# Performance work log

Measured on AMD Instinct MI355X. Metric: run time of the kernel, lower is better.

## Reference

```python
import jax, jax.numpy as jnp
import numpy as np

HIDDEN = 256
GAMMA = 0.96875
SCALE_BASE = 512


def _rotate_every_two(x):
    x1 = x[..., ::2]
    x2 = x[..., 1::2]
    return jnp.stack((-x2, x1), axis=-1).reshape(x.shape)


def _xpos(x, downscale):
    # x: [B, H, L, D]; offset=0 path of XPOS._forward_impl
    L = x.shape[2]
    D = x.shape[-1]
    half = D // 2
    # buffer: (arange(0, D, 2) + 0.4*D) / (1.4*D)  -> [half]
    scale_vec = (jnp.arange(0, D, 2, dtype=jnp.float32) + 0.4 * D) / (1.4 * D)
    # scale ** (arange(L)/scale_base)[:, None] -> [L, half]
    exps = jnp.arange(L, dtype=jnp.float32) / SCALE_BASE
    scale = scale_vec[None, :] ** exps[:, None]
    # fixed_pos_embedding on scale (dim = half)
    inv_freq = 1.0 / (10000.0 ** (jnp.arange(half, dtype=jnp.float32) / half))
    sinusoid = jnp.arange(L, dtype=jnp.float32)[:, None] * inv_freq[None, :]  # [L, half]
    sin = jnp.sin(sinusoid)
    cos = jnp.cos(sinusoid)
    if downscale:
        scale = 1.0 / scale
    sin2 = jnp.repeat(sin * scale, 2, axis=-1)  # duplicate_interleave -> [L, D]
    cos2 = jnp.repeat(cos * scale, 2, axis=-1)
    return x * cos2 + _rotate_every_two(x) * sin2


def _decay_mask(L):
    n = jnp.arange(L)[:, None]
    m = jnp.arange(L)[None, :]
    return jnp.where(n >= m, jnp.power(GAMMA, (n - m).astype(jnp.float32)), 0.0)


def setup_inputs() -> dict:
    key = jax.random.key(0)
    k1, k2, k3, k4 = jax.random.split(key, 4)
    B, H, L, D = 8, 4, 2048, HIDDEN
    X = jax.random.normal(k1, (B, H, L, D), dtype=jnp.float32)
    W_Q = jax.random.normal(k2, (D, D), dtype=jnp.float32) / D
    W_K = jax.random.normal(k3, (D, D), dtype=jnp.float32) / D
    W_V = jax.random.normal(k4, (D, D), dtype=jnp.float32) / D
    return {"X": X, "W_Q": W_Q, "W_K": W_K, "W_V": W_V}


def reference(X, W_Q, W_K, W_V):
    L = X.shape[2]
    Q = X @ W_Q
    K = X @ W_K
    Q = _xpos(Q, downscale=False)
    K = _xpos(K, downscale=True)
    V = X @ W_V
    D = _decay_mask(L)  # [L, L]
    att = jnp.einsum('bhnd,bhmd->bhnm', Q, K) * D[None, None]
    return att @ V
```

## Files before the change

### kernel.cpp

```cpp
#include <hip/hip_runtime.h>
#include <stdint.h>

typedef unsigned short u16;
typedef unsigned int   u32;
typedef __attribute__((ext_vector_type(8))) short  bf16x8;
typedef __attribute__((ext_vector_type(4))) float  f32x4;
typedef __attribute__((ext_vector_type(4))) u32    u32x4;
typedef __attribute__((ext_vector_type(2))) u32    u32x2;

#define L_SEQ 2048
#define DMODEL 256

__device__ __forceinline__ u16 f2bf(float x){
  u32 u = __float_as_uint(x);
  return (u16)((u + 0x7FFFu + ((u >> 16) & 1u)) >> 16);
}

__device__ __forceinline__ u32 pack2(float a, float b){
  return (u32)f2bf(a) | ((u32)f2bf(b) << 16);
}

__device__ __forceinline__ void gload_lds16(const void* g, void* l){
  __builtin_amdgcn_global_load_lds(
      (const __attribute__((address_space(1))) u32*)g,
      (__attribute__((address_space(3))) u32*)l, 16, 0, 0);
}

__global__ void k_tables(float2* __restrict__ tq2, float2* __restrict__ tk2){
  int idx = blockIdx.x * 256 + threadIdx.x;
  int n = idx >> 7, hi = idx & 127;
  float fn = (float)n, fi = (float)hi;
  float invf = exp2f(-(fi * (1.0f/128.0f)) * 13.2877124f);
  float ang = fn * invf;
  float s = sinf(ang), c = cosf(ang);
  float sv = (2.0f * fi + 102.4f) * (1.0f / 358.4f);
  float sc = exp2f((fn * (1.0f/512.0f)) * log2f(sv));
  float2 q; q.x = c * sc;  q.y = s * sc;
  tq2[idx] = q;
  float inv = 1.0f / sc;
  float2 k; k.x = c * inv; k.y = s * inv;
  tk2[idx] = k;
}

__global__ void k_wt(const float* __restrict__ wq, const float* __restrict__ wk,
                     const float* __restrict__ wv, u16* __restrict__ wt2){
  int idx = blockIdx.x * 256 + threadIdx.x;
  int kc = idx / 6144, r = idx % 6144;
  int col = r >> 3, p = r & 7;
  int j = p ^ (col & 7);
  int wsel = col >> 8, c = col & 255;
  const float* src = (wsel == 0) ? wq : ((wsel == 1) ? wk : wv);
  int k0 = kc * 64 + j * 8;
  u32x4 v;
  v.x = pack2(src[(k0+0)*256 + c], src[(k0+1)*256 + c]);
  v.y = pack2(src[(k0+2)*256 + c], src[(k0+3)*256 + c]);
  v.z = pack2(src[(k0+4)*256 + c], src[(k0+5)*256 + c]);
  v.w = pack2(src[(k0+6)*256 + c], src[(k0+7)*256 + c]);
  *(u32x4*)(wt2 + (size_t)idx * 8) = v;
}

__global__ void k_xbf(const float* __restrict__ X, u16* __restrict__ Xb2){
  int idx = blockIdx.x * 256 + threadIdx.x;
  int row = idx >> 5, g = idx & 31;
  int kc = g >> 3, j = g & 7;
  int p = j ^ (row & 7);
  const float4* src = (const float4*)(X + (size_t)row * 256 + g * 8);
  float4 a = src[0], b = src[1];
  u32x4 v;
  v.x = pack2(a.x, a.y); v.y = pack2(a.z, a.w);
  v.z = pack2(b.x, b.y); v.w = pack2(b.z, b.w);
  *(u32x4*)(Xb2 + (((size_t)kc * 65536 + row) * 8 + p) * 8) = v;
}

__global__ __launch_bounds__(256, 2) void k_proj(
    const u16* __restrict__ Xb2, const u16* __restrict__ Wt2,
    const float2* __restrict__ tq2, const float2* __restrict__ tk2,
    u16* __restrict__ Qx, u16* __restrict__ Kx, u16* __restrict__ VT)
{
  __shared__ char smem[65536];
  const int p0 = blockIdx.x;
  const int l = (p0 & 7) * 384 + (p0 >> 3);
  const int ct = l % 6;
  const int rt = l / 6;
  const int wsel = ct >> 1;
  const int mcol0 = (ct & 1) * 128;
  const int row0 = rt * 128;
  const int bh = rt >> 4;
  const int tid = threadIdx.x;
  const int lane = tid & 63, wid = tid >> 6;
  const int h = lane >> 4, l15 = lane & 15;
  const int wrg = wid >> 1, wcg = wid & 1;

  f32x4 acc[4][4] = {};

  auto stage = [&](int kc, int buf){
    const u16* xsrc = Xb2 + ((size_t)kc * 65536 + row0) * 64;
    const u16* wsrc = Wt2 + ((size_t)kc * 768 + ct * 128) * 64;
    char* xdst = smem + buf * 16384;
    char* wdst = smem + 32768 + buf * 16384;
#pragma unroll
    for (int t = 0; t < 4; ++t){
      int ci = t * 256 + tid;
      gload_lds16(xsrc + ci * 8, xdst + (t * 256 + wid * 64) * 16);
      gload_lds16(wsrc + ci * 8, wdst + (t * 256 + wid * 64) * 16);
    }
  };

  stage(0, 0);
  __syncthreads();

  for (int kc = 0; kc < 4; ++kc){
    const int cur = kc & 1;
    if (kc < 3) stage(kc + 1, cur ^ 1);

    const char* lX = smem + cur * 16384;
    const char* lW = smem + 32768 + cur * 16384;
#pragma unroll
    for (int kb = 0; kb < 2; ++kb){
      bf16x8 xf[4], wf[4];
#pragma unroll
      for (int b = 0; b < 4; ++b){
        int r = wrg * 64 + b * 16 + l15;
        int p = (kb * 4 + h) ^ (r & 7);
        xf[b] = *(const bf16x8*)(lX + r * 128 + p * 16);
      }
#pragma unroll
      for (int a = 0; a < 4; ++a){
        int c = wcg * 64 + a * 16 + l15;
        int p = (kb * 4 + h) ^ (c & 7);
        wf[a] = *(const bf16x8*)(lW + c * 128 + p * 16);
      }
      if (wsel < 2){
#pragma unroll
        for (int a = 0; a < 4; ++a)
#pragma unroll
          for (int b = 0; b < 4; ++b)
            acc[a][b] = __builtin_amdgcn_mfma_f32_16x16x32_bf16(
                wf[a], xf[b], acc[a][b], 0, 0, 0);
      } else {
#pragma unroll
        for (int b = 0; b < 4; ++b)
#pragma unroll
          for (int a = 0; a < 4; ++a)
            acc[b][a] = __builtin_amdgcn_mfma_f32_16x16x32_bf16(
                xf[b], wf[a], acc[b][a], 0, 0, 0);
      }
    }
    __syncthreads();
  }

  if (wsel < 2){
    const float2* tt = (wsel == 0) ? tq2 : tk2;
    u16* Od = (wsel == 0) ? Qx : Kx;
#pragma unroll
    for (int a = 0; a < 4; ++a){
      int d0 = mcol0 + wcg * 64 + a * 16 + h * 4;
#pragma unroll
      for (int b = 0; b < 4; ++b){
        int n = row0 + wrg * 64 + b * 16 + l15;
        int pos = n & 2047;
        f32x4 v = acc[a][b];
        float4 t = *(const float4*)(tt + pos * 128 + (d0 >> 1));
        float y0 = v.x * t.x - v.y * t.y;
        float y1 = v.y * t.x + v.x * t.y;
        float y2 = v.z * t.z - v.w * t.w;
        float y3 = v.w * t.z + v.z * t.w;
        u32x2 p2; p2.x = pack2(y0, y1); p2.y = pack2(y2, y3);
        int lrow = wrg * 64 + b * 16 + l15;
        int lcolb = (wcg * 64 + a * 16 + h * 4) * 2;
        *(u32x2*)(smem + lrow * 256 + (lcolb ^ ((lrow & 7) << 4))) = p2;
      }
    }
    __syncthreads();
    {
      const int r = tid >> 1;
      const int cbase = (tid & 1) * 8;
      u16* orow = Od + (size_t)(row0 + r) * 256 + mcol0 + cbase * 8;
#pragma unroll
      for (int j = 0; j < 8; ++j){
        int c16 = cbase + j;
        u32x4 v = *(const u32x4*)(smem + r * 256 +
                                  ((c16 * 16) ^ ((r & 7) << 4)));
        *(u32x4*)(orow + j * 8) = v;
      }
    }
  } else {
#pragma unroll
    for (int b = 0; b < 4; ++b){
      int lpos = wrg * 64 + b * 16 + h * 4;
#pragma unroll
      for (int a = 0; a < 4; ++a){
        int ld = wcg * 64 + a * 16 + l15;
        f32x4 v = acc[b][a];
        u32x2 p2; p2.x = pack2(v.x, v.y); p2.y = pack2(v.z, v.w);
        *(u32x2*)(smem + ld * 256 + ((lpos * 2) ^ ((ld & 7) << 4))) = p2;
      }
    }
    __syncthreads();
    {
      const int dloc = tid >> 1;
      const int cbase = (tid & 1) * 8;
      const int posbase = (rt & 15) * 128;
      u16* orow = VT + ((size_t)bh * DMODEL + mcol0 + dloc) * 2048 +
                  posbase + cbase * 8;
#pragma unroll
      for (int j = 0; j < 8; ++j){
        int c16 = cbase + j;
        u32x4 v = *(const u32x4*)(smem + dloc * 256 +
                                  ((c16 * 16) ^ ((dloc & 7) << 4)));
        *(u32x4*)(orow + j * 8) = v;
      }
    }
  }
}

__global__ __launch_bounds__(512) void k_attn(
    const u16* __restrict__ Qx, const u16* __restrict__ Kx,
    const u16* __restrict__ VT, float* __restrict__ out)
{
  __shared__ char smem[131072];

  const int pbid = blockIdx.x;
  const int bid = ((pbid & 7) << 6) | (pbid >> 3);
  const int bh = bid >> 4, i = bid & 15;
  const int tid = threadIdx.x;
  const int lane = tid & 63, w = tid >> 6;
  const int h = lane >> 4, l15 = lane & 15;
  const int n_g = i * 128 + w * 16 + l15;

  bf16x8 q[8];
  const u16* qbase = Qx + ((size_t)bh * 2048 + n_g) * 256;
#pragma unroll
  for (int kb = 0; kb < 8; ++kb)
    q[kb] = *(const bf16x8*)(qbase + kb * 32 + h * 8);

  f32x4 ot[16] = {};

  int j_lo = 2 * i - 4; if (j_lo < 0) j_lo = 0;
  const int j_hi = 2 * i + 1;
  const float L2G = -0.04580369f;
  const float GI1 = 1.03225806f;
  const float GI2 = 1.06555671f;
  const float GI3 = 1.09993040f;

  auto stage = [&](int j, int buf){
    const u16* kbase = Kx + ((size_t)bh * 2048 + j * 64) * 256;
    char* kdst = smem + buf * 32768;
#pragma unroll
    for (int t = 0; t < 4; ++t){
      int s = (w * 4 + t) * 64 + lane;
      int m = s >> 5, c = s & 31;
      gload_lds16(kbase + m * 256 + ((c ^ (m & 7)) * 8),
                  kdst + (w * 4 + t) * 1024);
    }
    const u16* vbase = VT + (size_t)bh * (DMODEL * 2048) + j * 64;
    char* vdst = smem + 65536 + buf * 32768;
#pragma unroll
    for (int t = 0; t < 4; ++t){
      int s = (w * 4 + t) * 64 + lane;
      int d = s >> 3, c = s & 7;
      gload_lds16(vbase + (size_t)d * 2048 + ((c ^ (d & 7)) * 8),
                  vdst + (w * 4 + t) * 1024);
    }
  };

  stage(j_lo, 0);
  __syncthreads();

  for (int j = j_lo; j <= j_hi; ++j){
    const int cur = (j - j_lo) & 1;
    if (j < j_hi) stage(j + 1, cur ^ 1);

    if (i * 128 + w * 16 + 15 >= j * 64){
      const char* ldsK = smem + cur * 32768;
      const char* ldsV = smem + 65536 + cur * 32768;
      f32x4 sacc[4] = {};
#pragma unroll
      for (int kb = 0; kb < 8; ++kb){
#pragma unroll
        for (int mt = 0; mt < 4; ++mt){
          int m = mt * 16 + l15;
          int chunk = kb * 4 + h;
          bf16x8 a = *(const bf16x8*)(ldsK + m * 512 +
                                      ((chunk ^ (m & 7)) * 16));
          sacc[mt] = __builtin_amdgcn_mfma_f32_16x16x32_bf16(
              a, q[kb], sacc[mt], 0, 0, 0);
        }
      }
      u32 dA[4], dB[4];
#pragma unroll
      for (int mt = 0; mt < 4; ++mt){
        int m0 = j * 64 + mt * 16 + h * 4;
        int dl = n_g - m0;
        float base = exp2f((float)dl * L2G);
        float v0 = (dl     >= 0) ? sacc[mt].x * base       : 0.0f;
        float v1 = (dl - 1 >= 0) ? sacc[mt].y * base * GI1 : 0.0f;
        float v2 = (dl - 2 >= 0) ? sacc[mt].z * base * GI2 : 0.0f;
        float v3 = (dl - 3 >= 0) ? sacc[mt].w * base * GI3 : 0.0f;
        dA[mt] = pack2(v0, v1);
        dB[mt] = pack2(v2, v3);
      }
      int s0 = l15 + 32 * (h & 1);
      int s1 = s0 + 16;
      bool lo = (h < 2);
#pragma unroll
      for (int kt = 0; kt < 2; ++kt){
        u32 a0 = (u32)__shfl((int)dA[2 * kt],     s0, 64);
        u32 a1 = (u32)__shfl((int)dA[2 * kt + 1], s0, 64);
        u32 b0 = (u32)__shfl((int)dB[2 * kt],     s0, 64);
        u32 b1 = (u32)__shfl((int)dB[2 * kt + 1], s0, 64);
        u32 a2 = (u32)__shfl((int)dA[2 * kt],     s1, 64);
        u32 a3 = (u32)__shfl((int)dA[2 * kt + 1], s1, 64);
        u32 b2 = (u32)__shfl((int)dB[2 * kt],     s1, 64);
        u32 b3 = (u32)__shfl((int)dB[2 * kt + 1], s1, 64);
        union { u32 u[4]; bf16x8 v; } uu;
        uu.u[0] = lo ? a0 : a1;
        uu.u[1] = lo ? b0 : b1;
        uu.u[2] = lo ? a2 : a3;
        uu.u[3] = lo ? b2 : b3;
        bf16x8 bfrag = uu.v;
#pragma unroll
        for (int dt = 0; dt < 16; ++dt){
          int d = dt * 16 + l15;
          int chunk = kt * 4 + h;
          bf16x8 a = *(const bf16x8*)(ldsV + d * 128 +
                                      ((chunk ^ (d & 7)) * 16));
          ot[dt] = __builtin_amdgcn_mfma_f32_16x16x32_bf16(
              a, bfrag, ot[dt], 0, 0, 0);
        }
      }
    }
    __syncthreads();
  }

  float* obase = out + ((size_t)bh * 2048 + n_g) * 256;
#pragma unroll
  for (int dt = 0; dt < 16; ++dt)
    *(f32x4*)(obase + dt * 16 + h * 4) = ot[dt];
}

extern "C" void kernel_launch(void* const* d_in, const int* in_sizes, int n_in,
                              void* d_out, int out_size, void* d_ws, size_t ws_size,
                              hipStream_t stream)
{
  (void)in_sizes; (void)n_in; (void)out_size; (void)ws_size;
  const float* X  = (const float*)d_in[0];
  const float* WQ = (const float*)d_in[1];
  const float* WK = (const float*)d_in[2];
  const float* WV = (const float*)d_in[3];
  float* out = (float*)d_out;

  char* ws = (char*)d_ws;
  float2* tq2 = (float2*)ws;
  float2* tk2 = (float2*)(ws + (2u << 20));
  u16* wt2 = (u16*)(ws + (4u << 20));
  u16* qx = (u16*)(ws + 4718592);
  u16* kx = (u16*)(ws + 38273024);
  u16* vt = (u16*)(ws + 71827456);

  u16* xb2 = (u16*)d_out;

  k_tables<<<dim3(1024), dim3(256), 0, stream>>>(tq2, tk2);
  k_wt<<<dim3(96), dim3(256), 0, stream>>>(WQ, WK, WV, wt2);
  k_xbf<<<dim3(8192), dim3(256), 0, stream>>>(X, xb2);
  k_proj<<<dim3(3072), dim3(256), 0, stream>>>(xb2, wt2, tq2, tk2, qx, kx, vt);
  k_attn<<<dim3(512), dim3(512), 0, stream>>>(qx, kx, vt, out);
}
```

Baseline: 143.8 us.

## Keep X tile resident in LDS and compute Q, K, V projections per block

The projection kernel now launches one 512-thread block per 128-row tile. The block loads the full 128x256 X tile into LDS once and loops over the Q, K and V weight matrices, streaming double-buffered 256-column weight chunks, instead of having six blocks each reload X for one 128-column slice. This removes redundant X reads from global memory but uses 128KB of LDS and leaves far fewer blocks for latency hiding. Separately, the attention kernel raises wave priority around its MFMA loops with s_setprio.

```diff
diff --git a/kernel.cpp b/kernel.cpp
--- a/kernel.cpp
+++ b/kernel.cpp
@@ -72,145 +72,150 @@
   *(u32x4*)(Xb2 + (((size_t)kc * 65536 + row) * 8 + p) * 8) = v;
 }
 
-__global__ __launch_bounds__(256, 2) void k_proj(
+__global__ __launch_bounds__(512, 2) void k_proj(
     const u16* __restrict__ Xb2, const u16* __restrict__ Wt2,
     const float2* __restrict__ tq2, const float2* __restrict__ tk2,
     u16* __restrict__ Qx, u16* __restrict__ Kx, u16* __restrict__ VT)
 {
-  __shared__ char smem[65536];
-  const int p0 = blockIdx.x;
-  const int l = (p0 & 7) * 384 + (p0 >> 3);
-  const int ct = l % 6;
-  const int rt = l / 6;
-  const int wsel = ct >> 1;
-  const int mcol0 = (ct & 1) * 128;
+  __shared__ char smem[131072];
+  const int rt = blockIdx.x;
   const int row0 = rt * 128;
   const int bh = rt >> 4;
   const int tid = threadIdx.x;
   const int lane = tid & 63, wid = tid >> 6;
   const int h = lane >> 4, l15 = lane & 15;
-  const int wrg = wid >> 1, wcg = wid & 1;
-
-  f32x4 acc[4][4] = {};
-
-  auto stage = [&](int kc, int buf){
+  const int wrg = wid >> 2, wcg = wid & 3;
+
+  char* const E = smem + 65536;
+
+  auto stageW = [&](int wsel, int kc, int buf){
+    const u16* wsrc = Wt2 + ((size_t)kc * 768 + wsel * 256) * 64;
+    char* dst = E + buf * 32768;
+#pragma unroll
+    for (int t = 0; t < 4; ++t){
+      int ci = t * 512 + tid;
+      gload_lds16(wsrc + ci * 8, dst + (t * 512 + wid * 64) * 16);
+    }
+  };
+
+#pragma unroll
+  for (int kc = 0; kc < 4; ++kc){
     const u16* xsrc = Xb2 + ((size_t)kc * 65536 + row0) * 64;
-    const u16* wsrc = Wt2 + ((size_t)kc * 768 + ct * 128) * 64;
-    char* xdst = smem + buf * 16384;
-    char* wdst = smem + 32768 + buf * 16384;
-#pragma unroll
-    for (int t = 0; t < 4; ++t){
-      int ci = t * 256 + tid;
-      gload_lds16(xsrc + ci * 8, xdst + (t * 256 + wid * 64) * 16);
-      gload_lds16(wsrc + ci * 8, wdst + (t * 256 + wid * 64) * 16);
-    }
-  };
-
-  stage(0, 0);
+#pragma unroll
+    for (int t = 0; t < 2; ++t){
+      int ci = t * 512 + tid;
+      gload_lds16(xsrc + ci * 8, smem + kc * 16384 + (t * 512 + wid * 64) * 16);
+    }
+  }
+  stageW(0, 0, 0);
   __syncthreads();
 
-  for (int kc = 0; kc < 4; ++kc){
-    const int cur = kc & 1;
-    if (kc < 3) stage(kc + 1, cur ^ 1);
-
-    const char* lX = smem + cur * 16384;
-    const char* lW = smem + 32768 + cur * 16384;
-#pragma unroll
-    for (int kb = 0; kb < 2; ++kb){
-      bf16x8 xf[4], wf[4];
+#pragma unroll
+  for (int wsel = 0; wsel < 3; ++wsel){
+    f32x4 acc[4][4] = {};
+
+    for (int kc = 0; kc < 4; ++kc){
+      const int cur = kc & 1;
+      if (kc < 3) stageW(wsel, kc + 1, cur ^ 1);
+      const char* lX = smem + kc * 16384;
+      const char* lW = E + cur * 32768;
+#pragma unroll
+      for (int kb = 0; kb < 2; ++kb){
+        bf16x8 xf[4], wf[4];
+#pragma unroll
+        for (int b = 0; b < 4; ++b){
+          int r = wrg * 64 + b * 16 + l15;
+          int p = (kb * 4 + h) ^ (r & 7);
+          xf[b] = *(const bf16x8*)(lX + r * 128 + p * 16);
+        }
+#pragma unroll
+        for (int a = 0; a < 4; ++a){
+          int c = wcg * 64 + a * 16 + l15;
+          int p = (kb * 4 + h) ^ (c & 7);
+          wf[a] = *(const bf16x8*)(lW + c * 128 + p * 16);
+        }
+        if (wsel < 2){
+#pragma unroll
+          for (int a = 0; a < 4; ++a)
+#pragma unroll
+            for (int b = 0; b < 4; ++b)
+              acc[a][b] = __builtin_amdgcn_mfma_f32_16x16x32_bf16(
+                  wf[a], xf[b], acc[a][b], 0, 0, 0);
+        } else {
+#pragma unroll
+          for (int b = 0; b < 4; ++b)
+#pragma unroll
+            for (int a = 0; a < 4; ++a)
+              acc[b][a] = __builtin_amdgcn_mfma_f32_16x16x32_bf16(
+                  xf[b], wf[a], acc[b][a], 0, 0, 0);
+        }
+      }
+      __syncthreads();
+    }
+
+    if (wsel < 2){
+      const float2* tt = (wsel == 0) ? tq2 : tk2;
+      u16* Od = (wsel == 0) ? Qx : Kx;
+#pragma unroll
+      for (int a = 0; a < 4; ++a){
+        int d0 = wcg * 64 + a * 16 + h * 4;
+#pragma unroll
+        for (int b = 0; b < 4; ++b){
+          int n = row0 + wrg * 64 + b * 16 + l15;
+          int pos = n & 2047;
+          f32x4 v = acc[a][b];
+          float4 t = *(const float4*)(tt + pos * 128 + (d0 >> 1));
+          float y0 = v.x * t.x - v.y * t.y;
+          float y1 = v.y * t.x + v.x * t.y;
+          float y2 = v.z * t.z - v.w * t.w;
+          float y3 = v.w * t.z + v.z * t.w;
+          u32x2 p2; p2.x = pack2(y0, y1); p2.y = pack2(y2, y3);
+          int lrow = wrg * 64 + b * 16 + l15;
+          *(u32x2*)(E + lrow * 512 + ((d0 * 2) ^ ((lrow & 7) << 4))) = p2;
+        }
+      }
+      __syncthreads();
+      {
+        const int r = tid >> 2;
+        const int q4 = tid & 3;
+        u16* orow = Od + (size_t)(row0 + r) * 256 + q4 * 64;
+#pragma unroll
+        for (int j = 0; j < 8; ++j){
+          int c = q4 * 8 + j;
+          u32x4 v = *(const u32x4*)(E + r * 512 +
+                                    ((c * 16) ^ ((r & 7) << 4)));
+          *(u32x4*)(orow + j * 8) = v;
+        }
+      }
+    } else {
 #pragma unroll
       for (int b = 0; b < 4; ++b){
-        int r = wrg * 64 + b * 16 + l15;
-        int p = (kb * 4 + h) ^ (r & 7);
-        xf[b] = *(const bf16x8*)(lX + r * 128 + p * 16);
-      }
-#pragma unroll
-      for (int a = 0; a < 4; ++a){
-        int c = wcg * 64 + a * 16 + l15;
-        int p = (kb * 4 + h) ^ (c & 7);
-        wf[a] = *(const bf16x8*)(lW + c * 128 + p * 16);
-      }
-      if (wsel < 2){
-#pragma unroll
-        for (int a = 0; a < 4; ++a)
-#pragma unroll
-          for (int b = 0; b < 4; ++b)
-            acc[a][b] = __builtin_amdgcn_mfma_f32_16x16x32_bf16(
-                wf[a], xf[b], acc[a][b], 0, 0, 0);
-      } else {
-#pragma unroll
-        for (int b = 0; b < 4; ++b)
-#pragma unroll
-          for (int a = 0; a < 4; ++a)
-            acc[b][a] = __builtin_amdgcn_mfma_f32_16x16x32_bf16(
-                xf[b], wf[a], acc[b][a], 0, 0, 0);
+        int lpos = wrg * 64 + b * 16 + h * 4;
+#pragma unroll
+        for (int a = 0; a < 4; ++a){
+          int ld = wcg * 64 + a * 16 + l15;
+          f32x4 v = acc[b][a];
+          u32x2 p2; p2.x = pack2(v.x, v.y); p2.y = pack2(v.z, v.w);
+          *(u32x2*)(E + ld * 256 + ((lpos * 2) ^ ((ld & 7) << 4))) = p2;
+        }
+      }
+      __syncthreads();
+      {
+        const int d = tid >> 1;
+        const int half = tid & 1;
+        u16* orow = VT + ((size_t)bh * DMODEL + d) * 2048 +
+                    (rt & 15) * 128 + half * 64;
+#pragma unroll
+        for (int j = 0; j < 8; ++j){
+          int c = half * 8 + j;
+          u32x4 v = *(const u32x4*)(E + d * 256 +
+                                    ((c * 16) ^ ((d & 7) << 4)));
+          *(u32x4*)(orow + j * 8) = v;
+        }
       }
     }
     __syncthreads();
-  }
-
-  if (wsel < 2){
-    const float2* tt = (wsel == 0) ? tq2 : tk2;
-    u16* Od = (wsel == 0) ? Qx : Kx;
-#pragma unroll
-    for (int a = 0; a < 4; ++a){
-      int d0 = mcol0 + wcg * 64 + a * 16 + h * 4;
-#pragma unroll
-      for (int b = 0; b < 4; ++b){
-        int n = row0 + wrg * 64 + b * 16 + l15;
-        int pos = n & 2047;
-        f32x4 v = acc[a][b];
-        float4 t = *(const float4*)(tt + pos * 128 + (d0 >> 1));
-        float y0 = v.x * t.x - v.y * t.y;
-        float y1 = v.y * t.x + v.x * t.y;
-        float y2 = v.z * t.z - v.w * t.w;
-        float y3 = v.w * t.z + v.z * t.w;
-        u32x2 p2; p2.x = pack2(y0, y1); p2.y = pack2(y2, y3);
-        int lrow = wrg * 64 + b * 16 + l15;
-        int lcolb = (wcg * 64 + a * 16 + h * 4) * 2;
-        *(u32x2*)(smem + lrow * 256 + (lcolb ^ ((lrow & 7) << 4))) = p2;
-      }
-    }
-    __syncthreads();
-    {
-      const int r = tid >> 1;
-      const int cbase = (tid & 1) * 8;
-      u16* orow = Od + (size_t)(row0 + r) * 256 + mcol0 + cbase * 8;
-#pragma unroll
-      for (int j = 0; j < 8; ++j){
-        int c16 = cbase + j;
-        u32x4 v = *(const u32x4*)(smem + r * 256 +
-                                  ((c16 * 16) ^ ((r & 7) << 4)));
-        *(u32x4*)(orow + j * 8) = v;
-      }
-    }
-  } else {
-#pragma unroll
-    for (int b = 0; b < 4; ++b){
-      int lpos = wrg * 64 + b * 16 + h * 4;
-#pragma unroll
-      for (int a = 0; a < 4; ++a){
-        int ld = wcg * 64 + a * 16 + l15;
-        f32x4 v = acc[b][a];
-        u32x2 p2; p2.x = pack2(v.x, v.y); p2.y = pack2(v.z, v.w);
-        *(u32x2*)(smem + ld * 256 + ((lpos * 2) ^ ((ld & 7) << 4))) = p2;
-      }
-    }
-    __syncthreads();
-    {
-      const int dloc = tid >> 1;
-      const int cbase = (tid & 1) * 8;
-      const int posbase = (rt & 15) * 128;
-      u16* orow = VT + ((size_t)bh * DMODEL + mcol0 + dloc) * 2048 +
-                  posbase + cbase * 8;
-#pragma unroll
-      for (int j = 0; j < 8; ++j){
-        int c16 = cbase + j;
-        u32x4 v = *(const u32x4*)(smem + dloc * 256 +
-                                  ((c16 * 16) ^ ((dloc & 7) << 4)));
-        *(u32x4*)(orow + j * 8) = v;
-      }
-    }
+    if (wsel < 2){ stageW(wsel + 1, 0, 0); __syncthreads(); }
   }
 }
 
@@ -275,6 +280,7 @@
       const char* ldsK = smem + cur * 32768;
       const char* ldsV = smem + 65536 + cur * 32768;
       f32x4 sacc[4] = {};
+      __builtin_amdgcn_s_setprio(1);
 #pragma unroll
       for (int kb = 0; kb < 8; ++kb){
 #pragma unroll
@@ -287,6 +293,7 @@
               a, q[kb], sacc[mt], 0, 0, 0);
         }
       }
+      __builtin_amdgcn_s_setprio(0);
       u32 dA[4], dB[4];
 #pragma unroll
       for (int mt = 0; mt < 4; ++mt){
@@ -319,6 +326,7 @@
         uu.u[2] = lo ? a2 : a3;
         uu.u[3] = lo ? b2 : b3;
         bf16x8 bfrag = uu.v;
+        __builtin_amdgcn_s_setprio(1);
 #pragma unroll
         for (int dt = 0; dt < 16; ++dt){
           int d = dt * 16 + l15;
@@ -328,6 +336,7 @@
           ot[dt] = __builtin_amdgcn_mfma_f32_16x16x32_bf16(
               a, bfrag, ot[dt], 0, 0, 0);
         }
+        __builtin_amdgcn_s_setprio(0);
       }
     }
     __syncthreads();
@@ -363,6 +372,6 @@
   k_tables<<<dim3(1024), dim3(256), 0, stream>>>(tq2, tk2);
   k_wt<<<dim3(96), dim3(256), 0, stream>>>(WQ, WK, WV, wt2);
   k_xbf<<<dim3(8192), dim3(256), 0, stream>>>(X, xb2);
-  k_proj<<<dim3(3072), dim3(256), 0, stream>>>(xb2, wt2, tq2, tk2, qx, kx, vt);
+  k_proj<<<dim3(512), dim3(512), 0, stream>>>(xb2, wt2, tq2, tk2, qx, kx, vt);
   k_attn<<<dim3(512), dim3(512), 0, stream>>>(qx, kx, vt, out);
 }
```

Result: slower. 157.7 us (+9.7%).

## Shrink projection K-chunks to 32 for higher occupancy; add MFMA priority in attention

Applied to the files above, without the earlier changes.

The projection kernel now stages 32-wide K chunks instead of 64, halving its LDS footprint to 32 KB. This raises the launch-bounds occupancy hint from 2 to 5 blocks. The pre-pass kernels re-pack X and the weights to match the new 4-chunk swizzle layout. The attention kernel wraps its MFMA loops in s_setprio to favour matrix issue over other waves. The cost is twice as many sync/stage iterations in the projection kernel, plus possible register pressure from the tighter bound.

```diff
diff --git a/kernel.cpp b/kernel.cpp
--- a/kernel.cpp
+++ b/kernel.cpp
@@ -43,41 +43,41 @@
 }
 
 __global__ void k_wt(const float* __restrict__ wq, const float* __restrict__ wk,
-                     const float* __restrict__ wv, u16* __restrict__ wt2){
+                     const float* __restrict__ wv, u16* __restrict__ wt3){
   int idx = blockIdx.x * 256 + threadIdx.x;
-  int kc = idx / 6144, r = idx % 6144;
-  int col = r >> 3, p = r & 7;
-  int j = p ^ (col & 7);
+  int kc = idx / 3072, r = idx % 3072;
+  int col = r >> 2, p = r & 3;
+  int j = p ^ ((col >> 1) & 3);
   int wsel = col >> 8, c = col & 255;
   const float* src = (wsel == 0) ? wq : ((wsel == 1) ? wk : wv);
-  int k0 = kc * 64 + j * 8;
+  int k0 = kc * 32 + j * 8;
   u32x4 v;
   v.x = pack2(src[(k0+0)*256 + c], src[(k0+1)*256 + c]);
   v.y = pack2(src[(k0+2)*256 + c], src[(k0+3)*256 + c]);
   v.z = pack2(src[(k0+4)*256 + c], src[(k0+5)*256 + c]);
   v.w = pack2(src[(k0+6)*256 + c], src[(k0+7)*256 + c]);
-  *(u32x4*)(wt2 + (size_t)idx * 8) = v;
-}
-
-__global__ void k_xbf(const float* __restrict__ X, u16* __restrict__ Xb2){
+  *(u32x4*)(wt3 + (size_t)idx * 8) = v;
+}
+
+__global__ void k_xbf(const float* __restrict__ X, u16* __restrict__ Xb3){
   int idx = blockIdx.x * 256 + threadIdx.x;
   int row = idx >> 5, g = idx & 31;
-  int kc = g >> 3, j = g & 7;
-  int p = j ^ (row & 7);
+  int kc = g >> 2, j = g & 3;
+  int p = j ^ ((row >> 1) & 3);
   const float4* src = (const float4*)(X + (size_t)row * 256 + g * 8);
   float4 a = src[0], b = src[1];
   u32x4 v;
   v.x = pack2(a.x, a.y); v.y = pack2(a.z, a.w);
   v.z = pack2(b.x, b.y); v.w = pack2(b.z, b.w);
-  *(u32x4*)(Xb2 + (((size_t)kc * 65536 + row) * 8 + p) * 8) = v;
-}
-
-__global__ __launch_bounds__(256, 2) void k_proj(
-    const u16* __restrict__ Xb2, const u16* __restrict__ Wt2,
+  *(u32x4*)(Xb3 + (((size_t)kc * 65536 + row) * 4 + p) * 8) = v;
+}
+
+__global__ __launch_bounds__(256, 5) void k_proj(
+    const u16* __restrict__ Xb3, const u16* __restrict__ Wt3,
     const float2* __restrict__ tq2, const float2* __restrict__ tk2,
     u16* __restrict__ Qx, u16* __restrict__ Kx, u16* __restrict__ VT)
 {
-  __shared__ char smem[65536];
+  __shared__ char smem[32768];
   const int p0 = blockIdx.x;
   const int l = (p0 & 7) * 384 + (p0 >> 3);
   const int ct = l % 6;
@@ -94,12 +94,12 @@
   f32x4 acc[4][4] = {};
 
   auto stage = [&](int kc, int buf){
-    const u16* xsrc = Xb2 + ((size_t)kc * 65536 + row0) * 64;
-    const u16* wsrc = Wt2 + ((size_t)kc * 768 + ct * 128) * 64;
-    char* xdst = smem + buf * 16384;
-    char* wdst = smem + 32768 + buf * 16384;
-#pragma unroll
-    for (int t = 0; t < 4; ++t){
+    const u16* xsrc = Xb3 + ((size_t)kc * 65536 + row0) * 32;
+    const u16* wsrc = Wt3 + ((size_t)kc * 768 + ct * 128) * 32;
+    char* xdst = smem + buf * 8192;
+    char* wdst = smem + 16384 + buf * 8192;
+#pragma unroll
+    for (int t = 0; t < 2; ++t){
       int ci = t * 256 + tid;
       gload_lds16(xsrc + ci * 8, xdst + (t * 256 + wid * 64) * 16);
       gload_lds16(wsrc + ci * 8, wdst + (t * 256 + wid * 64) * 16);
@@ -109,42 +109,39 @@
   stage(0, 0);
   __syncthreads();
 
-  for (int kc = 0; kc < 4; ++kc){
+  for (int kc = 0; kc < 8; ++kc){
     const int cur = kc & 1;
-    if (kc < 3) stage(kc + 1, cur ^ 1);
-
-    const char* lX = smem + cur * 16384;
-    const char* lW = smem + 32768 + cur * 16384;
-#pragma unroll
-    for (int kb = 0; kb < 2; ++kb){
-      bf16x8 xf[4], wf[4];
-#pragma unroll
-      for (int b = 0; b < 4; ++b){
-        int r = wrg * 64 + b * 16 + l15;
-        int p = (kb * 4 + h) ^ (r & 7);
-        xf[b] = *(const bf16x8*)(lX + r * 128 + p * 16);
-      }
-#pragma unroll
-      for (int a = 0; a < 4; ++a){
-        int c = wcg * 64 + a * 16 + l15;
-        int p = (kb * 4 + h) ^ (c & 7);
-        wf[a] = *(const bf16x8*)(lW + c * 128 + p * 16);
-      }
-      if (wsel < 2){
+    if (kc < 7) stage(kc + 1, cur ^ 1);
+
+    const char* lX = smem + cur * 8192;
+    const char* lW = smem + 16384 + cur * 8192;
+    bf16x8 xf[4], wf[4];
+#pragma unroll
+    for (int b = 0; b < 4; ++b){
+      int r = wrg * 64 + b * 16 + l15;
+      int p = h ^ ((r >> 1) & 3);
+      xf[b] = *(const bf16x8*)(lX + r * 64 + p * 16);
+    }
+#pragma unroll
+    for (int a = 0; a < 4; ++a){
+      int c = wcg * 64 + a * 16 + l15;
+      int p = h ^ ((c >> 1) & 3);
+      wf[a] = *(const bf16x8*)(lW + c * 64 + p * 16);
+    }
+    if (wsel < 2){
+#pragma unroll
+      for (int a = 0; a < 4; ++a)
+#pragma unroll
+        for (int b = 0; b < 4; ++b)
+          acc[a][b] = __builtin_amdgcn_mfma_f32_16x16x32_bf16(
+              wf[a], xf[b], acc[a][b], 0, 0, 0);
+    } else {
+#pragma unroll
+      for (int b = 0; b < 4; ++b)
 #pragma unroll
         for (int a = 0; a < 4; ++a)
-#pragma unroll
-          for (int b = 0; b < 4; ++b)
-            acc[a][b] = __builtin_amdgcn_mfma_f32_16x16x32_bf16(
-                wf[a], xf[b], acc[a][b], 0, 0, 0);
-      } else {
-#pragma unroll
-        for (int b = 0; b < 4; ++b)
-#pragma unroll
-          for (int a = 0; a < 4; ++a)
-            acc[b][a] = __builtin_amdgcn_mfma_f32_16x16x32_bf16(
-                xf[b], wf[a], acc[b][a], 0, 0, 0);
-      }
+          acc[b][a] = __builtin_amdgcn_mfma_f32_16x16x32_bf16(
+              xf[b], wf[a], acc[b][a], 0, 0, 0);
     }
     __syncthreads();
   }
@@ -275,6 +272,7 @@
       const char* ldsK = smem + cur * 32768;
       const char* ldsV = smem + 65536 + cur * 32768;
       f32x4 sacc[4] = {};
+      __builtin_amdgcn_s_setprio(1);
 #pragma unroll
       for (int kb = 0; kb < 8; ++kb){
 #pragma unroll
@@ -287,6 +285,7 @@
               a, q[kb], sacc[mt], 0, 0, 0);
         }
       }
+      __builtin_amdgcn_s_setprio(0);
       u32 dA[4], dB[4];
 #pragma unroll
       for (int mt = 0; mt < 4; ++mt){
@@ -319,6 +318,7 @@
         uu.u[2] = lo ? a2 : a3;
         uu.u[3] = lo ? b2 : b3;
         bf16x8 bfrag = uu.v;
+        __builtin_amdgcn_s_setprio(1);
 #pragma unroll
         for (int dt = 0; dt < 16; ++dt){
           int d = dt * 16 + l15;
@@ -328,6 +328,7 @@
           ot[dt] = __builtin_amdgcn_mfma_f32_16x16x32_bf16(
               a, bfrag, ot[dt], 0, 0, 0);
         }
+        __builtin_amdgcn_s_setprio(0);
       }
     }
     __syncthreads();
@@ -353,16 +354,16 @@
   char* ws = (char*)d_ws;
   float2* tq2 = (float2*)ws;
   float2* tk2 = (float2*)(ws + (2u << 20));
-  u16* wt2 = (u16*)(ws + (4u << 20));
+  u16* wt3 = (u16*)(ws + (4u << 20));
   u16* qx = (u16*)(ws + 4718592);
   u16* kx = (u16*)(ws + 38273024);
   u16* vt = (u16*)(ws + 71827456);
 
-  u16* xb2 = (u16*)d_out;
+  u16* xb3 = (u16*)d_out;
 
   k_tables<<<dim3(1024), dim3(256), 0, stream>>>(tq2, tk2);
-  k_wt<<<dim3(96), dim3(256), 0, stream>>>(WQ, WK, WV, wt2);
-  k_xbf<<<dim3(8192), dim3(256), 0, stream>>>(X, xb2);
-  k_proj<<<dim3(3072), dim3(256), 0, stream>>>(xb2, wt2, tq2, tk2, qx, kx, vt);
+  k_wt<<<dim3(96), dim3(256), 0, stream>>>(WQ, WK, WV, wt3);
+  k_xbf<<<dim3(8192), dim3(256), 0, stream>>>(X, xb3);
+  k_proj<<<dim3(3072), dim3(256), 0, stream>>>(xb3, wt3, tq2, tk2, qx, kx, vt);
   k_attn<<<dim3(512), dim3(512), 0, stream>>>(qx, kx, vt, out);
 }
```

After: 422.3 us. +193.7%, slower.
